# Kernel tuning notes

Measured on AMD Instinct MI355X. Metric: run time of the kernel, lower is better.

Reference implementation:

```python
import jax, jax.numpy as jnp
import numpy as np

B, NUM_CLASSES, FEAT_DIM = 8192, 751, 2048
CLIP_LO, CLIP_HI = 1e-12, 1e12


def setup_inputs() -> dict:
    key = jax.random.key(0)
    kx, kl, kc = jax.random.split(key, 3)
    x = jax.random.normal(kx, (B, FEAT_DIM), dtype=jnp.float32)
    # labels are one-hot float rows, as fed to K.dot(labels, centers)
    idx = jax.random.randint(kl, (B,), 0, NUM_CLASSES)
    labels = jax.nn.one_hot(idx, NUM_CLASSES, dtype=jnp.float32)
    centers = jax.random.normal(kc, (NUM_CLASSES, FEAT_DIM), dtype=jnp.float32)
    return {"x": x, "labels": labels, "centers": centers}


def reference(x, labels, centers):
    # gathered class centers via dense one-hot matmul (faithful to K.dot)
    diff = x - jnp.dot(labels, centers)          # [B, feat_dim]
    per_sample = jnp.sum(diff * diff, axis=1)    # [B]
    per_sample = jnp.clip(per_sample, CLIP_LO, CLIP_HI)
    return jnp.mean(per_sample)
```

## Files before the change

### kernel.cpp

```cpp
#include <hip/hip_runtime.h>


#define BATCH 8192
#define NUM_CLASSES 751
#define FEAT_DIM 2048

__global__ __launch_bounds__(256) void center_loss_kernel(
    const float* __restrict__ x,
    const float* __restrict__ labels,
    const float* __restrict__ centers,
    float* __restrict__ partials)
{
    const int row = blockIdx.x;
    const int tid = threadIdx.x;

    const float4* __restrict__ xrow = (const float4*)(x + (size_t)row * FEAT_DIM);
    float4 xv0 = xrow[tid];
    float4 xv1 = xrow[tid + 256];

    __shared__ int s_idx;
    const float* lrow = labels + (size_t)row * NUM_CLASSES;
    #pragma unroll
    for (int c = tid; c < NUM_CLASSES; c += 256) {
        if (lrow[c] > 0.5f) s_idx = c;
    }
    __syncthreads();
    const int idx = s_idx;

    const float4* __restrict__ crow = (const float4*)(centers + (size_t)idx * FEAT_DIM);
    float4 cv0 = crow[tid];
    float4 cv1 = crow[tid + 256];

    float dx = xv0.x - cv0.x, dy = xv0.y - cv0.y, dz = xv0.z - cv0.z, dw = xv0.w - cv0.w;
    float sum = dx * dx + dy * dy + dz * dz + dw * dw;
    dx = xv1.x - cv1.x; dy = xv1.y - cv1.y; dz = xv1.z - cv1.z; dw = xv1.w - cv1.w;
    sum += dx * dx + dy * dy + dz * dz + dw * dw;

    #pragma unroll
    for (int off = 32; off > 0; off >>= 1)
        sum += __shfl_down(sum, off, 64);

    __shared__ float s_part[4];
    const int wave = tid >> 6;
    const int lane = tid & 63;
    if (lane == 0) s_part[wave] = sum;
    __syncthreads();

    if (tid == 0) {
        float ps = s_part[0] + s_part[1] + s_part[2] + s_part[3];
        ps = fminf(fmaxf(ps, 1e-12f), 1e12f);
        partials[row] = ps;
    }
}

__global__ __launch_bounds__(256) void reduce_kernel(
    const float* __restrict__ partials,
    float* __restrict__ out)
{
    const int tid = threadIdx.x;
    const float4* __restrict__ p4 = (const float4*)partials;

    float sum = 0.0f;
    #pragma unroll
    for (int k = 0; k < 8; ++k) {
        float4 v = p4[tid + 256 * k];
        sum += v.x + v.y + v.z + v.w;
    }

    #pragma unroll
    for (int off = 32; off > 0; off >>= 1)
        sum += __shfl_down(sum, off, 64);

    __shared__ float s_part[4];
    const int wave = tid >> 6;
    const int lane = tid & 63;
    if (lane == 0) s_part[wave] = sum;
    __syncthreads();

    if (tid == 0) {
        float total = s_part[0] + s_part[1] + s_part[2] + s_part[3];
        out[0] = total * (1.0f / (float)BATCH);
    }
}

extern "C" void kernel_launch(void* const* d_in, const int* in_sizes, int n_in,
                              void* d_out, int out_size, void* d_ws, size_t ws_size,
                              hipStream_t stream)
{
    const float* x       = (const float*)d_in[0];
    const float* labels  = (const float*)d_in[1];
    const float* centers = (const float*)d_in[2];
    float* out      = (float*)d_out;
    float* partials = (float*)d_ws;

    center_loss_kernel<<<BATCH, 256, 0, stream>>>(x, labels, centers, partials);
    reduce_kernel<<<1, 256, 0, stream>>>(partials, out);
}
```

Baseline: 115.6 us.

## Assign one wavefront per row and drop block-level barriers

Each 64-lane wavefront now handles a whole row, with four rows per block, so the shared-memory label index and the __syncthreads calls go away. The label scan uses a wave-wide max shuffle to find the hot class. The x and label rows are read with nontemporal loads, issued up front before the center gather so more loads are in flight. Each lane now holds more registers (8 float4 plus 12 label floats), which may lower occupancy.

```diff
diff --git a/kernel.cpp b/kernel.cpp
--- a/kernel.cpp
+++ b/kernel.cpp
@@ -5,50 +5,60 @@
 #define NUM_CLASSES 751
 #define FEAT_DIM 2048
 
+typedef float fvec4 __attribute__((ext_vector_type(4)));
+
 __global__ __launch_bounds__(256) void center_loss_kernel(
     const float* __restrict__ x,
     const float* __restrict__ labels,
     const float* __restrict__ centers,
     float* __restrict__ partials)
 {
-    const int row = blockIdx.x;
-    const int tid = threadIdx.x;
+    const int wave = threadIdx.x >> 6;
+    const int lane = threadIdx.x & 63;
+    const int row  = (blockIdx.x << 2) + wave;
 
-    const float4* __restrict__ xrow = (const float4*)(x + (size_t)row * FEAT_DIM);
-    float4 xv0 = xrow[tid];
-    float4 xv1 = xrow[tid + 256];
+    const float* __restrict__ lrow = labels + (size_t)row * NUM_CLASSES;
+    float lv[12];
+    #pragma unroll
+    for (int k = 0; k < 11; ++k)
+        lv[k] = __builtin_nontemporal_load(&lrow[lane + 64 * k]);
+    lv[11] = (lane < NUM_CLASSES - 704)
+                 ? __builtin_nontemporal_load(&lrow[704 + lane]) : 0.0f;
 
-    __shared__ int s_idx;
-    const float* lrow = labels + (size_t)row * NUM_CLASSES;
+    const fvec4* __restrict__ xrow = (const fvec4*)(x + (size_t)row * FEAT_DIM);
+    fvec4 xv[8];
     #pragma unroll
-    for (int c = tid; c < NUM_CLASSES; c += 256) {
-        if (lrow[c] > 0.5f) s_idx = c;
+    for (int k = 0; k < 8; ++k)
+        xv[k] = __builtin_nontemporal_load(&xrow[lane + 64 * k]);
+
+    int myidx = -1;
+    #pragma unroll
+    for (int k = 0; k < 12; ++k)
+        if (lv[k] > 0.5f) myidx = lane + 64 * k;
+    #pragma unroll
+    for (int off = 32; off > 0; off >>= 1) {
+        int other = __shfl_xor(myidx, off, 64);
+        myidx = myidx > other ? myidx : other;
     }
-    __syncthreads();
-    const int idx = s_idx;
 
-    const float4* __restrict__ crow = (const float4*)(centers + (size_t)idx * FEAT_DIM);
-    float4 cv0 = crow[tid];
-    float4 cv1 = crow[tid + 256];
-
-    float dx = xv0.x - cv0.x, dy = xv0.y - cv0.y, dz = xv0.z - cv0.z, dw = xv0.w - cv0.w;
-    float sum = dx * dx + dy * dy + dz * dz + dw * dw;
-    dx = xv1.x - cv1.x; dy = xv1.y - cv1.y; dz = xv1.z - cv1.z; dw = xv1.w - cv1.w;
-    sum += dx * dx + dy * dy + dz * dz + dw * dw;
+    const fvec4* __restrict__ crow = (const fvec4*)(centers + (size_t)myidx * FEAT_DIM);
+    float sum = 0.0f;
+    #pragma unroll
+    for (int k = 0; k < 8; ++k) {
+        fvec4 cv = crow[lane + 64 * k];
+        float dx = xv[k].x - cv.x;
+        float dy = xv[k].y - cv.y;
+        float dz = xv[k].z - cv.z;
+        float dw = xv[k].w - cv.w;
+        sum += dx * dx + dy * dy + dz * dz + dw * dw;
+    }
 
     #pragma unroll
     for (int off = 32; off > 0; off >>= 1)
-        sum += __shfl_down(sum, off, 64);
+        sum += __shfl_xor(sum, off, 64);
 
-    __shared__ float s_part[4];
-    const int wave = tid >> 6;
-    const int lane = tid & 63;
-    if (lane == 0) s_part[wave] = sum;
-    __syncthreads();
-
-    if (tid == 0) {
-        float ps = s_part[0] + s_part[1] + s_part[2] + s_part[3];
-        ps = fminf(fmaxf(ps, 1e-12f), 1e12f);
+    if (lane == 0) {
+        float ps = fminf(fmaxf(sum, 1e-12f), 1e12f);
         partials[row] = ps;
     }
 }
@@ -58,18 +68,18 @@
     float* __restrict__ out)
 {
     const int tid = threadIdx.x;
-    const float4* __restrict__ p4 = (const float4*)partials;
+    const fvec4* __restrict__ p4 = (const fvec4*)partials;
 
     float sum = 0.0f;
     #pragma unroll
     for (int k = 0; k < 8; ++k) {
-        float4 v = p4[tid + 256 * k];
+        fvec4 v = p4[tid + 256 * k];
         sum += v.x + v.y + v.z + v.w;
     }
 
     #pragma unroll
     for (int off = 32; off > 0; off >>= 1)
-        sum += __shfl_down(sum, off, 64);
+        sum += __shfl_xor(sum, off, 64);
 
     __shared__ float s_part[4];
     const int wave = tid >> 6;
@@ -93,6 +103,6 @@
     float* out      = (float*)d_out;
     float* partials = (float*)d_ws;
 
-    center_loss_kernel<<<BATCH, 256, 0, stream>>>(x, labels, centers, partials);
+    center_loss_kernel<<<BATCH / 4, 256, 0, stream>>>(x, labels, centers, partials);
     reduce_kernel<<<1, 256, 0, stream>>>(partials, out);
 }
```

New measurement: 122.3 us. 5.7% more time.
